# Performance work log

Measured on AMD Instinct MI355X. Metric: run time of the kernel, lower is better.

The kernel has to match this reference:

```python
import jax, jax.numpy as jnp
import numpy as np

N_TOKENS = 7168
EMBED_DIM = 256
N_HEADS = 8
HEAD_DIM = EMBED_DIM // N_HEADS  # 32
HALF = HEAD_DIM // 2             # 16 rotary frequency pairs per head
BATCH = 4
MAX_LEN = 2048
POSITION_DIM = 2
N_LEVELS = 4
LN_EPS = 1e-5
SPATIAL_THETA = 100.0
LEVEL_THETA = 10.0


def setup_inputs() -> dict:
    key = jax.random.key(0)
    ks = jax.random.split(key, 6)
    x = jax.random.normal(ks[0], (N_TOKENS, EMBED_DIM), jnp.float32)
    level_indices = jax.random.randint(ks[1], (N_TOKENS,), 0, N_LEVELS, dtype=jnp.int32)
    level_spatial_shapes = jnp.array([[32, 32], [16, 16], [8, 8], [4, 4]], jnp.int32)
    # positions in each token's own level coordinate space
    u = jax.random.uniform(ks[2], (N_TOKENS, POSITION_DIM), jnp.float32)
    spatial_positions = u * level_spatial_shapes[level_indices].astype(jnp.float32)
    # ragged batch boundaries: lengths [2048, 1536, 2048, 1536]
    batch_offsets = jnp.array([0, 2048, 3584, 5632, 7168], jnp.int32)
    ln_w = jnp.ones((EMBED_DIM,), jnp.float32)
    ln_b = jnp.zeros((EMBED_DIM,), jnp.float32)
    qkv_w = jax.random.normal(ks[3], (3 * EMBED_DIM, EMBED_DIM), jnp.float32) * (EMBED_DIM ** -0.5)
    out_w = jax.random.normal(ks[4], (EMBED_DIM, EMBED_DIM), jnp.float32) * (EMBED_DIM ** -0.5)
    # ND-RoPE frequencies: (position_dim+1, n_heads, head_dim//2).
    # Spatial dims share magnitude theta_s^(-i/HALF) split over a random per-head
    # direction angle; level dim uses theta_l^(-i/HALF).
    mag_s = SPATIAL_THETA ** (-jnp.arange(HALF, dtype=jnp.float32) / HALF)
    mag_l = LEVEL_THETA ** (-jnp.arange(HALF, dtype=jnp.float32) / HALF)
    phi = jax.random.uniform(ks[5], (N_HEADS, HALF), jnp.float32) * (2.0 * jnp.pi)
    freqs = jnp.stack([mag_s * jnp.cos(phi),
                       mag_s * jnp.sin(phi),
                       jnp.broadcast_to(mag_l, (N_HEADS, HALF))], axis=0)
    return {"x": x, "spatial_positions": spatial_positions,
            "level_indices": level_indices, "level_spatial_shapes": level_spatial_shapes,
            "batch_offsets": batch_offsets, "ln_w": ln_w, "ln_b": ln_b,
            "qkv_w": qkv_w, "out_w": out_w, "freqs": freqs}


def reference(x, spatial_positions, level_indices, level_spatial_shapes,
              batch_offsets, ln_w, ln_b, qkv_w, out_w, freqs):
    residual = x
    # pre-norm LayerNorm
    mu = jnp.mean(x, -1, keepdims=True)
    var = jnp.mean((x - mu) ** 2, -1, keepdims=True)
    xn = (x - mu) * jax.lax.rsqrt(var + LN_EPS) * ln_w + ln_b
    q, k, v = jnp.split(xn @ qkv_w.T, 3, axis=-1)  # each (N, E)
    # prep_multilevel_positions: rescale each level to the max level's coordinate
    # frame and append the level index as an extra position dim.
    shapes_tok = level_spatial_shapes[level_indices].astype(jnp.float32)  # (N, 2)
    max_shape = jnp.max(level_spatial_shapes, axis=0).astype(jnp.float32)  # (2,)
    pos = jnp.concatenate([spatial_positions * (max_shape / shapes_tok),
                           level_indices[:, None].astype(jnp.float32)], axis=-1)  # (N, 3)
    # per-head ND RoPE: angle = sum_d pos_d * freq_d
    theta = jnp.einsum('nd,dhf->nhf', pos, freqs)  # (N, H, HALF)
    cos, sin = jnp.cos(theta), jnp.sin(theta)

    def rope(t):
        t = t.reshape(N_TOKENS, N_HEADS, HALF, 2)
        r = jnp.stack([t[..., 0] * cos - t[..., 1] * sin,
                       t[..., 0] * sin + t[..., 1] * cos], axis=-1)
        return r.reshape(N_TOKENS, EMBED_DIM)

    q, k = rope(q), rope(k)
    # concatenated -> padded (B, S, E)
    tok = jnp.arange(N_TOKENS)
    b_of = jnp.searchsorted(batch_offsets, tok, side='right') - 1  # (N,) batch index
    p_of = tok - batch_offsets[b_of]                               # (N,) pos in batch
    lens = batch_offsets[1:] - batch_offsets[:-1]
    pad_mask = jnp.arange(MAX_LEN)[None, :] >= lens[:, None]  # (B, S), True = padding

    def heads(t):
        padded = jnp.zeros((BATCH, MAX_LEN, EMBED_DIM), t.dtype).at[b_of, p_of].set(t)
        return padded.reshape(BATCH, MAX_LEN, N_HEADS, HEAD_DIM).transpose(0, 2, 1, 3)

    qh, kh, vh = heads(q), heads(k), heads(v)  # (B, H, S, hd)
    scores = jnp.einsum('bhqd,bhkd->bhqk', qh, kh) / np.float32(np.sqrt(HEAD_DIM))
    scores = jnp.where(pad_mask[:, None, None, :], jnp.float32(-1e9), scores)
    attn = jax.nn.softmax(scores, axis=-1)
    out = jnp.einsum('bhqk,bhkd->bhqd', attn, vh)
    out = out.transpose(0, 2, 1, 3).reshape(BATCH, MAX_LEN, EMBED_DIM)
    out_cat = out[b_of, p_of]  # padded -> concatenated (padded rows dropped)
    return out_cat @ out_w.T + residual
```

## Files before the change

### kernel.cpp

```cpp
#include <hip/hip_runtime.h>
#include <hip/hip_bf16.h>

#define NT   7168
#define ED   256
#define NH   8
#define HD   32
#define HF   16
#define QKVN 768
#define QSCL 0.25503471600819466f

typedef float f32x4  __attribute__((ext_vector_type(4)));
typedef __bf16 bf16x8 __attribute__((ext_vector_type(8)));

__device__ __forceinline__ short f2bf(float f) {
    union { float f; unsigned u; } v; v.f = f;
    unsigned r = v.u + 0x7FFFu + ((v.u >> 16) & 1u);
    return (short)(r >> 16);
}
__device__ __forceinline__ float fexp2(float x) {
    float r; asm("v_exp_f32 %0, %1" : "=v"(r) : "v"(x)); return r;
}
__device__ __forceinline__ unsigned cvtpk(float lo, float hi) {
    unsigned r; asm("v_cvt_pk_bf16_f32 %0, %1, %2" : "=v"(r) : "v"(lo), "v"(hi)); return r;
}
__device__ __forceinline__ float bf2f(short s) {
    union { unsigned u; float f; } v; v.u = ((unsigned)(unsigned short)s) << 16;
    return v.f;
}
__device__ __forceinline__ unsigned pack2bf(float a, float b) {
    union { float f; unsigned u; } ua, ub; ua.f = a; ub.f = b;
    return ((ua.u + 0x8000u) >> 16) | ((ub.u + 0x8000u) & 0xFFFF0000u);
}
__device__ __forceinline__ void gll16(const void* g, void* l) {
    __builtin_amdgcn_global_load_lds((const __attribute__((address_space(1))) void*)g,
                                     (__attribute__((address_space(3))) void*)l, 16, 0, 0);
}

__global__ __launch_bounds__(256) void ln_conv_kernel(const float* __restrict__ x,
                                                      const float* __restrict__ w,
                                                      const float* __restrict__ b,
                                                      short* __restrict__ xn,
                                                      const float* __restrict__ qkvw,
                                                      const float* __restrict__ outw,
                                                      short* __restrict__ wq,
                                                      short* __restrict__ wo,
                                                      const float* __restrict__ sp,
                                                      const int* __restrict__ lvl,
                                                      const int* __restrict__ shp,
                                                      const float* __restrict__ freqs,
                                                      unsigned* __restrict__ tab) {
    int bid = blockIdx.x;
    int tid = threadIdx.x;
    if (bid >= NT / 4) {
        int i = (bid - NT / 4) * 256 + tid;
        if (i < QKVN * ED) wq[i] = f2bf(qkvw[i]);
        if (i < ED * ED)   wo[i] = f2bf(outw[i]);
        return;
    }
    int tok  = bid * 4 + (tid >> 6);
    int lane = tid & 63;
    const float4 xv = *reinterpret_cast<const float4*>(x + tok * ED + lane * 4);
    float s  = xv.x + xv.y + xv.z + xv.w;
    float ss = xv.x * xv.x + xv.y * xv.y + xv.z * xv.z + xv.w * xv.w;
#pragma unroll
    for (int m = 1; m < 64; m <<= 1) { s += __shfl_xor(s, m); ss += __shfl_xor(ss, m); }
    float mu  = s * (1.0f / ED);
    float inv = rsqrtf(ss * (1.0f / ED) - mu * mu + 1e-5f);
    const float4 wv = *reinterpret_cast<const float4*>(w + lane * 4);
    const float4 bv = *reinterpret_cast<const float4*>(b + lane * 4);
    short4 o;
    o.x = f2bf((xv.x - mu) * inv * wv.x + bv.x);
    o.y = f2bf((xv.y - mu) * inv * wv.y + bv.y);
    o.z = f2bf((xv.z - mu) * inv * wv.z + bv.z);
    o.w = f2bf((xv.w - mu) * inv * wv.w + bv.w);
    *reinterpret_cast<short4*>(xn + tok * ED + lane * 4) = o;

    int tt = bid * 4 + (tid >> 6);
    int h  = (tid >> 3) & 7;
    int f  = (tid & 7) * 2;
    int L = lvl[tt];
    float mx0 = fmaxf(fmaxf((float)shp[0], (float)shp[2]), fmaxf((float)shp[4], (float)shp[6]));
    float mx1 = fmaxf(fmaxf((float)shp[1], (float)shp[3]), fmaxf((float)shp[5], (float)shp[7]));
    float p0 = sp[tt * 2]     * (mx0 / (float)shp[L * 2]);
    float p1 = sp[tt * 2 + 1] * (mx1 / (float)shp[L * 2 + 1]);
    float p2 = (float)L;
    int fi = h * HF + f;
    float th0 = p0 * freqs[fi]       + p1 * freqs[128 + fi]       + p2 * freqs[256 + fi];
    float th1 = p0 * freqs[fi + 1]   + p1 * freqs[128 + fi + 1]   + p2 * freqs[256 + fi + 1];
    float sn0, cs0, sn1, cs1;
    __sincosf(th0, &sn0, &cs0);
    __sincosf(th1, &sn1, &cs1);
    uint2 pk;
    pk.x = pack2bf(cs0, sn0);
    pk.y = pack2bf(cs1, sn1);
    *reinterpret_cast<uint2*>(&tab[tt * 128 + fi]) = pk;
}

__global__ __launch_bounds__(256) void gemm_qkv(const short* __restrict__ A,
                                                const short* __restrict__ B,
                                                short* __restrict__ C,
                                                const unsigned* __restrict__ tab,
                                                short* __restrict__ vt) {
    __shared__ __align__(16) short tile[4][2560];
    int wv = threadIdx.x >> 6, lane = threadIdx.x & 63;
    int r = lane & 15, g = lane >> 4;
    int mt = blockIdx.x * 128 + wv * 32;
    int jt = blockIdx.y * 64;
    const short* arow0 = A + (mt + r) * ED + g * 8;
    const short* arow1 = A + (mt + 16 + r) * ED + g * 8;
    const short* brow  = B + (jt + r) * ED + g * 8;
    f32x4 acc0[4] = {{0,0,0,0},{0,0,0,0},{0,0,0,0},{0,0,0,0}};
    f32x4 acc1[4] = {{0,0,0,0},{0,0,0,0},{0,0,0,0},{0,0,0,0}};
#pragma unroll
    for (int k0 = 0; k0 < ED; k0 += 32) {
        bf16x8 a0 = *reinterpret_cast<const bf16x8*>(arow0 + k0);
        bf16x8 a1 = *reinterpret_cast<const bf16x8*>(arow1 + k0);
#pragma unroll
        for (int c = 0; c < 4; ++c) {
            bf16x8 bb = *reinterpret_cast<const bf16x8*>(brow + c * 16 * ED + k0);
            acc0[c] = __builtin_amdgcn_mfma_f32_16x16x32_bf16(a0, bb, acc0[c], 0, 0, 0);
            acc1[c] = __builtin_amdgcn_mfma_f32_16x16x32_bf16(a1, bb, acc1[c], 0, 0, 0);
        }
    }
    short* tl = tile[wv];
    if (jt < 512) {
        const float qs = (jt < 256) ? QSCL : 1.0f;
        const int odd = r & 1;
#pragma unroll
        for (int c = 0; c < 4; ++c) {
            int col = jt + c * 16 + r;
            int hf = ((col >> 5) & 7) * 16 + ((col >> 1) & 15);
#pragma unroll
            for (int rr = 0; rr < 4; ++rr) {
                int t0 = mt + g * 4 + rr;
                unsigned pk0 = tab[t0 * 128 + hf];
                float cs0 = bf2f((short)(pk0 & 0xFFFF)), sn0 = bf2f((short)(pk0 >> 16));
                float v0 = acc0[c][rr], p0 = __shfl_xor(v0, 1);
                float o0 = (odd ? (v0 * cs0 + p0 * sn0) : (v0 * cs0 - p0 * sn0)) * qs;
                int t1 = t0 + 16;
                unsigned pk1 = tab[t1 * 128 + hf];
                float cs1 = bf2f((short)(pk1 & 0xFFFF)), sn1 = bf2f((short)(pk1 >> 16));
                float v1 = acc1[c][rr], p1 = __shfl_xor(v1, 1);
                float o1 = (odd ? (v1 * cs1 + p1 * sn1) : (v1 * cs1 - p1 * sn1)) * qs;
                float n0 = __shfl_xor(o0, 1);
                float n1 = __shfl_xor(o1, 1);
                int tok = (odd ? 16 : 0) + g * 4 + rr;
                unsigned dw = odd ? pack2bf(n1, o1) : pack2bf(o0, n0);
                int colw = c * 16 + (r & ~1);
                *reinterpret_cast<unsigned*>(&tl[tok * 72 + colw]) = dw;
            }
        }
#pragma unroll
        for (int p2 = 0; p2 < 4; ++p2) {
            int tok = p2 * 8 + (lane >> 3), chunk = lane & 7;
            uint4 d = *reinterpret_cast<const uint4*>(&tl[tok * 72 + chunk * 8]);
            *reinterpret_cast<uint4*>(&C[(size_t)(mt + tok) * QKVN + jt + chunk * 8]) = d;
        }
    } else {
#pragma unroll
        for (int c = 0; c < 4; ++c) {
            int row = c * 16 + r;
#pragma unroll
            for (int rr = 0; rr < 4; rr += 2) {
                unsigned d0 = pack2bf(acc0[c][rr], acc0[c][rr + 1]);
                unsigned d1 = pack2bf(acc1[c][rr], acc1[c][rr + 1]);
                *reinterpret_cast<unsigned*>(&tl[row * 40 + rr + 8 * g])     = d0;
                *reinterpret_cast<unsigned*>(&tl[row * 40 + rr + 4 + 8 * g]) = d1;
            }
        }
#pragma unroll
        for (int p2 = 0; p2 < 4; ++p2) {
            int dim = p2 * 16 + (lane >> 2), chunk = lane & 3;
            uint4 d = *reinterpret_cast<const uint4*>(&tl[dim * 40 + chunk * 8]);
            *reinterpret_cast<uint4*>(&vt[(size_t)(jt - 512 + dim) * NT + mt + chunk * 8]) = d;
        }
    }
}

__global__ __launch_bounds__(256) void gemm_out(const short* __restrict__ A,
                                                const short* __restrict__ B,
                                                const float* __restrict__ res,
                                                float* __restrict__ out) {
    int wv = threadIdx.x >> 6, lane = threadIdx.x & 63;
    int r = lane & 15, g = lane >> 4;
    int mt = blockIdx.x * 64 + wv * 16;
    int jt = blockIdx.y * 64;
    const short* arow = A + (mt + r) * ED + g * 8;
    const short* brow = B + (jt + r) * ED + g * 8;
    f32x4 acc[4] = {{0,0,0,0},{0,0,0,0},{0,0,0,0},{0,0,0,0}};
#pragma unroll
    for (int k0 = 0; k0 < ED; k0 += 32) {
        bf16x8 a = *reinterpret_cast<const bf16x8*>(arow + k0);
#pragma unroll
        for (int c = 0; c < 4; ++c) {
            bf16x8 bb = *reinterpret_cast<const bf16x8*>(brow + c * 16 * ED + k0);
            acc[c] = __builtin_amdgcn_mfma_f32_16x16x32_bf16(a, bb, acc[c], 0, 0, 0);
        }
    }
#pragma unroll
    for (int c = 0; c < 4; ++c)
#pragma unroll
        for (int rr = 0; rr < 4; ++rr) {
            int idx = (mt + g * 4 + rr) * ED + jt + c * 16 + r;
            out[idx] = acc[c][rr] + res[idx];
        }
}

__global__ __launch_bounds__(512) void attn_kernel(const short* __restrict__ qkv,
                                                   const short* __restrict__ vt,
                                                   short* __restrict__ obf) {
    __shared__ __align__(16) short smem[32768];
    const int tid = threadIdx.x;
    const int wv = tid >> 6, lane = tid & 63;
    const int bid = blockIdx.x;
    const int h = bid & 7, pr = bid >> 3;
    const int b = (pr >= 16) + (pr >= 28) + (pr >= 44);
    const int off = (b == 0) ? 0 : (b == 1) ? 2048 : (b == 2) ? 3584 : 5632;
    const int len = (b == 0) ? 2048 : (b == 1) ? 1536 : (b == 2) ? 2048 : 1536;
    const int pb  = (b == 0) ? 0 : (b == 1) ? 16 : (b == 2) ? 28 : 44;
    const int q0 = off + (pr - pb) * 128;
    const int r = lane & 15, g = lane >> 4;
    const int qi = wv & 3, half = wv >> 2;
    const int hl = len >> 1;
    const int nst = hl >> 7;
    const int qs = q0 + qi * 32;

    const int sh = tid >> 8, inner = tid & 255;
    const short* pK0 = qkv + ED + h * HD + (size_t)(off + sh * hl + (inner >> 2)) * QKVN + (inner & 3) * 8;
    const short* pV0 = vt + (size_t)(h * HD + ((inner >> 2) & 31)) * NT + off + sh * hl + (inner >> 7) * 32 + (inner & 3) * 8;
    const int dK0 = sh * 4096 + inner * 8;
    const int dK1 = sh * 4096 + (inner + 256) * 8;
    const int dV0 = 8192 + sh * 4096 + inner * 8;
    const int dV1 = 8192 + sh * 4096 + 2048 + inner * 8;

#define STAGE(B, s) { \
        const short* k_ = pK0 + (size_t)(s) * 128 * QKVN; \
        gll16(k_,             &smem[(B) * 16384 + dK0]); \
        gll16(k_ + 64 * QKVN, &smem[(B) * 16384 + dK1]); \
        const short* v_ = pV0 + (s) * 128; \
        gll16(v_,      &smem[(B) * 16384 + dV0]); \
        gll16(v_ + 64, &smem[(B) * 16384 + dV1]); }

    bf16x8 qfA = *reinterpret_cast<const bf16x8*>(qkv + (size_t)(qs + r) * QKVN + h * HD + g * 8);
    bf16x8 qfB = *reinterpret_cast<const bf16x8*>(qkv + (size_t)(qs + 16 + r) * QKVN + h * HD + g * 8);
    union { unsigned u[4]; bf16x8 v; } onesu;
    onesu.u[0] = onesu.u[1] = onesu.u[2] = onesu.u[3] = 0x3F803F80u;
    const bf16x8 ones = onesu.v;

    f32x4 o0A = {0,0,0,0}, o1A = {0,0,0,0}, o0B = {0,0,0,0}, o1B = {0,0,0,0};
    f32x4 olA = {0,0,0,0}, olB = {0,0,0,0};

    STAGE(0, 0);
    __syncthreads();

    for (int st = 0; st < nst; ++st) {
        const int Bb = st & 1;
        if (st + 1 < nst) STAGE(Bb ^ 1, st + 1);
#pragma unroll
        for (int sub = 0; sub < 2; ++sub) {
            const short* kl = &smem[Bb * 16384 + half * 4096 + sub * 2048];
            const short* vl = &smem[Bb * 16384 + 8192 + half * 4096 + sub * 2048];
            bf16x8 kf0 = *reinterpret_cast<const bf16x8*>(kl +        r * 32 + g * 8);
            bf16x8 kf1 = *reinterpret_cast<const bf16x8*>(kl +  512 + r * 32 + g * 8);
            bf16x8 kf2 = *reinterpret_cast<const bf16x8*>(kl + 1024 + r * 32 + g * 8);
            bf16x8 kf3 = *reinterpret_cast<const bf16x8*>(kl + 1536 + r * 32 + g * 8);
            bf16x8 v00 = *reinterpret_cast<const bf16x8*>(vl +        r * 32 + g * 8);
            bf16x8 v10 = *reinterpret_cast<const bf16x8*>(vl +  512 + r * 32 + g * 8);
            bf16x8 v01 = *reinterpret_cast<const bf16x8*>(vl + 1024 + r * 32 + g * 8);
            bf16x8 v11 = *reinterpret_cast<const bf16x8*>(vl + 1536 + r * 32 + g * 8);

            const f32x4 z = {0, 0, 0, 0};
            __builtin_amdgcn_s_setprio(1);
            f32x4 sA0 = __builtin_amdgcn_mfma_f32_16x16x32_bf16(kf0, qfA, z, 0, 0, 0);
            f32x4 sA1 = __builtin_amdgcn_mfma_f32_16x16x32_bf16(kf1, qfA, z, 0, 0, 0);
            f32x4 sA2 = __builtin_amdgcn_mfma_f32_16x16x32_bf16(kf2, qfA, z, 0, 0, 0);
            f32x4 sA3 = __builtin_amdgcn_mfma_f32_16x16x32_bf16(kf3, qfA, z, 0, 0, 0);
            f32x4 sB0 = __builtin_amdgcn_mfma_f32_16x16x32_bf16(kf0, qfB, z, 0, 0, 0);
            f32x4 sB1 = __builtin_amdgcn_mfma_f32_16x16x32_bf16(kf1, qfB, z, 0, 0, 0);
            f32x4 sB2 = __builtin_amdgcn_mfma_f32_16x16x32_bf16(kf2, qfB, z, 0, 0, 0);
            f32x4 sB3 = __builtin_amdgcn_mfma_f32_16x16x32_bf16(kf3, qfB, z, 0, 0, 0);
            __builtin_amdgcn_s_setprio(0);

#pragma unroll
            for (int i = 0; i < 4; ++i) {
                sA0[i] = fexp2(sA0[i]); sA1[i] = fexp2(sA1[i]);
                sA2[i] = fexp2(sA2[i]); sA3[i] = fexp2(sA3[i]);
                sB0[i] = fexp2(sB0[i]); sB1[i] = fexp2(sB1[i]);
                sB2[i] = fexp2(sB2[i]); sB3[i] = fexp2(sB3[i]);
            }
            union { unsigned u[4]; bf16x8 v; } pA0, pA1, pB0, pB1;
            pA0.u[0] = cvtpk(sA0[0], sA0[1]); pA0.u[1] = cvtpk(sA0[2], sA0[3]);
            pA0.u[2] = cvtpk(sA1[0], sA1[1]); pA0.u[3] = cvtpk(sA1[2], sA1[3]);
            pA1.u[0] = cvtpk(sA2[0], sA2[1]); pA1.u[1] = cvtpk(sA2[2], sA2[3]);
            pA1.u[2] = cvtpk(sA3[0], sA3[1]); pA1.u[3] = cvtpk(sA3[2], sA3[3]);
            pB0.u[0] = cvtpk(sB0[0], sB0[1]); pB0.u[1] = cvtpk(sB0[2], sB0[3]);
            pB0.u[2] = cvtpk(sB1[0], sB1[1]); pB0.u[3] = cvtpk(sB1[2], sB1[3]);
            pB1.u[0] = cvtpk(sB2[0], sB2[1]); pB1.u[1] = cvtpk(sB2[2], sB2[3]);
            pB1.u[2] = cvtpk(sB3[0], sB3[1]); pB1.u[3] = cvtpk(sB3[2], sB3[3]);
            __builtin_amdgcn_s_setprio(1);
            o0A = __builtin_amdgcn_mfma_f32_16x16x32_bf16(v00, pA0.v, o0A, 0, 0, 0);
            o0A = __builtin_amdgcn_mfma_f32_16x16x32_bf16(v01, pA1.v, o0A, 0, 0, 0);
            o1A = __builtin_amdgcn_mfma_f32_16x16x32_bf16(v10, pA0.v, o1A, 0, 0, 0);
            o1A = __builtin_amdgcn_mfma_f32_16x16x32_bf16(v11, pA1.v, o1A, 0, 0, 0);
            o0B = __builtin_amdgcn_mfma_f32_16x16x32_bf16(v00, pB0.v, o0B, 0, 0, 0);
            o0B = __builtin_amdgcn_mfma_f32_16x16x32_bf16(v01, pB1.v, o0B, 0, 0, 0);
            o1B = __builtin_amdgcn_mfma_f32_16x16x32_bf16(v10, pB0.v, o1B, 0, 0, 0);
            o1B = __builtin_amdgcn_mfma_f32_16x16x32_bf16(v11, pB1.v, o1B, 0, 0, 0);
            olA = __builtin_amdgcn_mfma_f32_16x16x32_bf16(ones, pA0.v, olA, 0, 0, 0);
            olA = __builtin_amdgcn_mfma_f32_16x16x32_bf16(ones, pA1.v, olA, 0, 0, 0);
            olB = __builtin_amdgcn_mfma_f32_16x16x32_bf16(ones, pB0.v, olB, 0, 0, 0);
            olB = __builtin_amdgcn_mfma_f32_16x16x32_bf16(ones, pB1.v, olB, 0, 0, 0);
            __builtin_amdgcn_s_setprio(0);
        }
        __syncthreads();
    }

    float lA = olA[0], lB = olB[0];

    float* cf = (float*)smem + (qi * 64 + lane) * 19;
    if (half) {
#pragma unroll
        for (int i = 0; i < 4; ++i) {
            cf[i] = o0A[i]; cf[4 + i] = o1A[i]; cf[8 + i] = o0B[i]; cf[12 + i] = o1B[i];
        }
        cf[16] = lA; cf[17] = lB;
    }
    __syncthreads();
    if (!half) {
        lA += cf[16]; lB += cf[17];
#pragma unroll
        for (int i = 0; i < 4; ++i) {
            o0A[i] += cf[i];     o1A[i] += cf[4 + i];
            o0B[i] += cf[8 + i]; o1B[i] += cf[12 + i];
        }
        float iA = 1.f / lA, iB = 1.f / lB;
        short4 w;
        short* orowA = obf + (qs + r) * ED + h * HD;
        w.x = f2bf(o0A[0] * iA); w.y = f2bf(o0A[1] * iA);
        w.z = f2bf(o0A[2] * iA); w.w = f2bf(o0A[3] * iA);
        *reinterpret_cast<short4*>(orowA + g * 4) = w;
        w.x = f2bf(o1A[0] * iA); w.y = f2bf(o1A[1] * iA);
        w.z = f2bf(o1A[2] * iA); w.w = f2bf(o1A[3] * iA);
        *reinterpret_cast<short4*>(orowA + 16 + g * 4) = w;
        short* orowB = obf + (qs + 16 + r) * ED + h * HD;
        w.x = f2bf(o0B[0] * iB); w.y = f2bf(o0B[1] * iB);
        w.z = f2bf(o0B[2] * iB); w.w = f2bf(o0B[3] * iB);
        *reinterpret_cast<short4*>(orowB + g * 4) = w;
        w.x = f2bf(o1B[0] * iB); w.y = f2bf(o1B[1] * iB);
        w.z = f2bf(o1B[2] * iB); w.w = f2bf(o1B[3] * iB);
        *reinterpret_cast<short4*>(orowB + 16 + g * 4) = w;
    }
#undef STAGE
}

extern "C" void kernel_launch(void* const* d_in, const int* in_sizes, int n_in,
                              void* d_out, int out_size, void* d_ws, size_t ws_size,
                              hipStream_t stream) {
    const float* x     = (const float*)d_in[0];
    const float* sp    = (const float*)d_in[1];
    const int*   lvl   = (const int*)d_in[2];
    const int*   shp   = (const int*)d_in[3];
    const float* lnw   = (const float*)d_in[5];
    const float* lnb   = (const float*)d_in[6];
    const float* qkvw  = (const float*)d_in[7];
    const float* outw  = (const float*)d_in[8];
    const float* freqs = (const float*)d_in[9];
    float* out = (float*)d_out;

    char* ws = (char*)d_ws;
    short* xn  = (short*)ws; ws += NT * ED * 2;
    short* qkv = (short*)ws; ws += NT * QKVN * 2;
    short* vt  = (short*)ws; ws += ED * NT * 2;
    short* obf = (short*)ws; ws += NT * ED * 2;
    short* wq  = (short*)ws; ws += QKVN * ED * 2;
    short* wo  = (short*)ws; ws += ED * ED * 2;
    unsigned* tab = (unsigned*)ws; ws += NT * 128 * 4;

    ln_conv_kernel<<<dim3(NT / 4 + 768), dim3(256), 0, stream>>>(
        x, lnw, lnb, xn, qkvw, outw, wq, wo, sp, lvl, shp, freqs, tab);
    gemm_qkv<<<dim3(NT / 128, QKVN / 64), dim3(256), 0, stream>>>(xn, wq, qkv, tab, vt);
    attn_kernel<<<dim3(56 * 8), dim3(512), 0, stream>>>(qkv, vt, obf);
    gemm_out<<<dim3(NT / 64, ED / 64), dim3(256), 0, stream>>>(obf, wo, x, out);
}
```

Measured before the change: 67.71 us.

## Re-split attention waves into 64-query tiles over key quarters with VALU row sums

The attention block now splits its 8 waves as 2 query groups of 64 rows times 4 key quarters, instead of 4 groups of 32 rows times 2 key halves. Each stage stages 64 keys, so every K/V fragment read from LDS feeds twice as many queries. The softmax denominator is now accumulated with VALU adds and cross-lane shuffles rather than extra MFMAs against a ones vector. The price is more accumulator registers per wave, a larger three-way LDS reduction at the end, and a min-occupancy launch bound that may constrain register allocation.

```diff
diff --git a/kernel.cpp b/kernel.cpp
--- a/kernel.cpp
+++ b/kernel.cpp
@@ -30,6 +30,9 @@
 __device__ __forceinline__ unsigned pack2bf(float a, float b) {
     union { float f; unsigned u; } ua, ub; ua.f = a; ub.f = b;
     return ((ua.u + 0x8000u) >> 16) | ((ub.u + 0x8000u) & 0xFFFF0000u);
+}
+__device__ __forceinline__ float vsum4(f32x4 v) {
+    return (v[0] + v[1]) + (v[2] + v[3]);
 }
 __device__ __forceinline__ void gll16(const void* g, void* l) {
     __builtin_amdgcn_global_load_lds((const __attribute__((address_space(1))) void*)g,
@@ -206,9 +209,9 @@
         }
 }
 
-__global__ __launch_bounds__(512) void attn_kernel(const short* __restrict__ qkv,
-                                                   const short* __restrict__ vt,
-                                                   short* __restrict__ obf) {
+__global__ __launch_bounds__(512, 4) void attn_kernel(const short* __restrict__ qkv,
+                                                      const short* __restrict__ vt,
+                                                      short* __restrict__ obf) {
     __shared__ __align__(16) short smem[32768];
     const int tid = threadIdx.x;
     const int wv = tid >> 6, lane = tid & 63;
@@ -220,35 +223,34 @@
     const int pb  = (b == 0) ? 0 : (b == 1) ? 16 : (b == 2) ? 28 : 44;
     const int q0 = off + (pr - pb) * 128;
     const int r = lane & 15, g = lane >> 4;
-    const int qi = wv & 3, half = wv >> 2;
-    const int hl = len >> 1;
-    const int nst = hl >> 7;
-    const int qs = q0 + qi * 32;
-
-    const int sh = tid >> 8, inner = tid & 255;
-    const short* pK0 = qkv + ED + h * HD + (size_t)(off + sh * hl + (inner >> 2)) * QKVN + (inner & 3) * 8;
-    const short* pV0 = vt + (size_t)(h * HD + ((inner >> 2) & 31)) * NT + off + sh * hl + (inner >> 7) * 32 + (inner & 3) * 8;
-    const int dK0 = sh * 4096 + inner * 8;
-    const int dK1 = sh * 4096 + (inner + 256) * 8;
-    const int dV0 = 8192 + sh * 4096 + inner * 8;
-    const int dV1 = 8192 + sh * 4096 + 2048 + inner * 8;
+    const int qi = wv & 1, qr = wv >> 1;
+    const int ql = len >> 2;
+    const int nst = ql >> 6;
+    const int qs = q0 + qi * 64;
+
+    const int qr_s = tid >> 7, inner = tid & 127;
+    const short* pK = qkv + ED + h * HD + (size_t)(off + qr_s * ql + (inner >> 2)) * QKVN + (inner & 3) * 8;
+    const short* pV = vt + (size_t)(h * HD + (inner >> 2)) * NT + off + qr_s * ql + (inner & 3) * 8;
+    const int dK = qr_s * 4096 + inner * 8;
+    const int dV = dK + 2048;
 
 #define STAGE(B, s) { \
-        const short* k_ = pK0 + (size_t)(s) * 128 * QKVN; \
-        gll16(k_,             &smem[(B) * 16384 + dK0]); \
-        gll16(k_ + 64 * QKVN, &smem[(B) * 16384 + dK1]); \
-        const short* v_ = pV0 + (s) * 128; \
-        gll16(v_,      &smem[(B) * 16384 + dV0]); \
-        gll16(v_ + 64, &smem[(B) * 16384 + dV1]); }
-
-    bf16x8 qfA = *reinterpret_cast<const bf16x8*>(qkv + (size_t)(qs + r) * QKVN + h * HD + g * 8);
-    bf16x8 qfB = *reinterpret_cast<const bf16x8*>(qkv + (size_t)(qs + 16 + r) * QKVN + h * HD + g * 8);
-    union { unsigned u[4]; bf16x8 v; } onesu;
-    onesu.u[0] = onesu.u[1] = onesu.u[2] = onesu.u[3] = 0x3F803F80u;
-    const bf16x8 ones = onesu.v;
-
-    f32x4 o0A = {0,0,0,0}, o1A = {0,0,0,0}, o0B = {0,0,0,0}, o1B = {0,0,0,0};
-    f32x4 olA = {0,0,0,0}, olB = {0,0,0,0};
+        const short* k_ = pK + (size_t)(s) * 64 * QKVN; \
+        gll16(k_,             &smem[(B) * 16384 + dK]); \
+        gll16(k_ + 32 * QKVN, &smem[(B) * 16384 + dK + 1024]); \
+        const short* v_ = pV + (s) * 64; \
+        gll16(v_,      &smem[(B) * 16384 + dV]); \
+        gll16(v_ + 32, &smem[(B) * 16384 + dV + 1024]); }
+
+    const short* qbase = qkv + (size_t)(qs + r) * QKVN + h * HD + g * 8;
+    bf16x8 qf0 = *reinterpret_cast<const bf16x8*>(qbase);
+    bf16x8 qf1 = *reinterpret_cast<const bf16x8*>(qbase + 16 * QKVN);
+    bf16x8 qf2 = *reinterpret_cast<const bf16x8*>(qbase + 32 * QKVN);
+    bf16x8 qf3 = *reinterpret_cast<const bf16x8*>(qbase + 48 * QKVN);
+
+    f32x4 o00 = {0,0,0,0}, o01 = {0,0,0,0}, o10 = {0,0,0,0}, o11 = {0,0,0,0};
+    f32x4 o20 = {0,0,0,0}, o21 = {0,0,0,0}, o30 = {0,0,0,0}, o31 = {0,0,0,0};
+    float l0 = 0.f, l1 = 0.f, l2 = 0.f, l3 = 0.f;
 
     STAGE(0, 0);
     __syncthreads();
@@ -256,31 +258,29 @@
     for (int st = 0; st < nst; ++st) {
         const int Bb = st & 1;
         if (st + 1 < nst) STAGE(Bb ^ 1, st + 1);
-#pragma unroll
-        for (int sub = 0; sub < 2; ++sub) {
-            const short* kl = &smem[Bb * 16384 + half * 4096 + sub * 2048];
-            const short* vl = &smem[Bb * 16384 + 8192 + half * 4096 + sub * 2048];
-            bf16x8 kf0 = *reinterpret_cast<const bf16x8*>(kl +        r * 32 + g * 8);
-            bf16x8 kf1 = *reinterpret_cast<const bf16x8*>(kl +  512 + r * 32 + g * 8);
-            bf16x8 kf2 = *reinterpret_cast<const bf16x8*>(kl + 1024 + r * 32 + g * 8);
-            bf16x8 kf3 = *reinterpret_cast<const bf16x8*>(kl + 1536 + r * 32 + g * 8);
-            bf16x8 v00 = *reinterpret_cast<const bf16x8*>(vl +        r * 32 + g * 8);
-            bf16x8 v10 = *reinterpret_cast<const bf16x8*>(vl +  512 + r * 32 + g * 8);
-            bf16x8 v01 = *reinterpret_cast<const bf16x8*>(vl + 1024 + r * 32 + g * 8);
-            bf16x8 v11 = *reinterpret_cast<const bf16x8*>(vl + 1536 + r * 32 + g * 8);
-
-            const f32x4 z = {0, 0, 0, 0};
+        const short* kl = &smem[Bb * 16384 + qr * 4096];
+        const short* vl = kl + 2048;
+        bf16x8 kf0 = *reinterpret_cast<const bf16x8*>(kl +        r * 32 + g * 8);
+        bf16x8 kf1 = *reinterpret_cast<const bf16x8*>(kl +  512 + r * 32 + g * 8);
+        bf16x8 kf2 = *reinterpret_cast<const bf16x8*>(kl + 1024 + r * 32 + g * 8);
+        bf16x8 kf3 = *reinterpret_cast<const bf16x8*>(kl + 1536 + r * 32 + g * 8);
+        bf16x8 v00 = *reinterpret_cast<const bf16x8*>(vl +        r * 32 + g * 8);
+        bf16x8 v10 = *reinterpret_cast<const bf16x8*>(vl +  512 + r * 32 + g * 8);
+        bf16x8 v01 = *reinterpret_cast<const bf16x8*>(vl + 1024 + r * 32 + g * 8);
+        bf16x8 v11 = *reinterpret_cast<const bf16x8*>(vl + 1536 + r * 32 + g * 8);
+        const f32x4 z = {0, 0, 0, 0};
+
+        {
             __builtin_amdgcn_s_setprio(1);
-            f32x4 sA0 = __builtin_amdgcn_mfma_f32_16x16x32_bf16(kf0, qfA, z, 0, 0, 0);
-            f32x4 sA1 = __builtin_amdgcn_mfma_f32_16x16x32_bf16(kf1, qfA, z, 0, 0, 0);
-            f32x4 sA2 = __builtin_amdgcn_mfma_f32_16x16x32_bf16(kf2, qfA, z, 0, 0, 0);
-            f32x4 sA3 = __builtin_amdgcn_mfma_f32_16x16x32_bf16(kf3, qfA, z, 0, 0, 0);
-            f32x4 sB0 = __builtin_amdgcn_mfma_f32_16x16x32_bf16(kf0, qfB, z, 0, 0, 0);
-            f32x4 sB1 = __builtin_amdgcn_mfma_f32_16x16x32_bf16(kf1, qfB, z, 0, 0, 0);
-            f32x4 sB2 = __builtin_amdgcn_mfma_f32_16x16x32_bf16(kf2, qfB, z, 0, 0, 0);
-            f32x4 sB3 = __builtin_amdgcn_mfma_f32_16x16x32_bf16(kf3, qfB, z, 0, 0, 0);
+            f32x4 sA0 = __builtin_amdgcn_mfma_f32_16x16x32_bf16(kf0, qf0, z, 0, 0, 0);
+            f32x4 sA1 = __builtin_amdgcn_mfma_f32_16x16x32_bf16(kf1, qf0, z, 0, 0, 0);
+            f32x4 sA2 = __builtin_amdgcn_mfma_f32_16x16x32_bf16(kf2, qf0, z, 0, 0, 0);
+            f32x4 sA3 = __builtin_amdgcn_mfma_f32_16x16x32_bf16(kf3, qf0, z, 0, 0, 0);
+            f32x4 sB0 = __builtin_amdgcn_mfma_f32_16x16x32_bf16(kf0, qf1, z, 0, 0, 0);
+            f32x4 sB1 = __builtin_amdgcn_mfma_f32_16x16x32_bf16(kf1, qf1, z, 0, 0, 0);
+            f32x4 sB2 = __builtin_amdgcn_mfma_f32_16x16x32_bf16(kf2, qf1, z, 0, 0, 0);
+            f32x4 sB3 = __builtin_amdgcn_mfma_f32_16x16x32_bf16(kf3, qf1, z, 0, 0, 0);
             __builtin_amdgcn_s_setprio(0);
-
 #pragma unroll
             for (int i = 0; i < 4; ++i) {
                 sA0[i] = fexp2(sA0[i]); sA1[i] = fexp2(sA1[i]);
@@ -288,6 +288,8 @@
                 sB0[i] = fexp2(sB0[i]); sB1[i] = fexp2(sB1[i]);
                 sB2[i] = fexp2(sB2[i]); sB3[i] = fexp2(sB3[i]);
             }
+            l0 += (vsum4(sA0) + vsum4(sA1)) + (vsum4(sA2) + vsum4(sA3));
+            l1 += (vsum4(sB0) + vsum4(sB1)) + (vsum4(sB2) + vsum4(sB3));
             union { unsigned u[4]; bf16x8 v; } pA0, pA1, pB0, pB1;
             pA0.u[0] = cvtpk(sA0[0], sA0[1]); pA0.u[1] = cvtpk(sA0[2], sA0[3]);
             pA0.u[2] = cvtpk(sA1[0], sA1[1]); pA0.u[3] = cvtpk(sA1[2], sA1[3]);
@@ -298,57 +300,103 @@
             pB1.u[0] = cvtpk(sB2[0], sB2[1]); pB1.u[1] = cvtpk(sB2[2], sB2[3]);
             pB1.u[2] = cvtpk(sB3[0], sB3[1]); pB1.u[3] = cvtpk(sB3[2], sB3[3]);
             __builtin_amdgcn_s_setprio(1);
-            o0A = __builtin_amdgcn_mfma_f32_16x16x32_bf16(v00, pA0.v, o0A, 0, 0, 0);
-            o0A = __builtin_amdgcn_mfma_f32_16x16x32_bf16(v01, pA1.v, o0A, 0, 0, 0);
-            o1A = __builtin_amdgcn_mfma_f32_16x16x32_bf16(v10, pA0.v, o1A, 0, 0, 0);
-            o1A = __builtin_amdgcn_mfma_f32_16x16x32_bf16(v11, pA1.v, o1A, 0, 0, 0);
-            o0B = __builtin_amdgcn_mfma_f32_16x16x32_bf16(v00, pB0.v, o0B, 0, 0, 0);
-            o0B = __builtin_amdgcn_mfma_f32_16x16x32_bf16(v01, pB1.v, o0B, 0, 0, 0);
-            o1B = __builtin_amdgcn_mfma_f32_16x16x32_bf16(v10, pB0.v, o1B, 0, 0, 0);
-            o1B = __builtin_amdgcn_mfma_f32_16x16x32_bf16(v11, pB1.v, o1B, 0, 0, 0);
-            olA = __builtin_amdgcn_mfma_f32_16x16x32_bf16(ones, pA0.v, olA, 0, 0, 0);
-            olA = __builtin_amdgcn_mfma_f32_16x16x32_bf16(ones, pA1.v, olA, 0, 0, 0);
-            olB = __builtin_amdgcn_mfma_f32_16x16x32_bf16(ones, pB0.v, olB, 0, 0, 0);
-            olB = __builtin_amdgcn_mfma_f32_16x16x32_bf16(ones, pB1.v, olB, 0, 0, 0);
+            o00 = __builtin_amdgcn_mfma_f32_16x16x32_bf16(v00, pA0.v, o00, 0, 0, 0);
+            o00 = __builtin_amdgcn_mfma_f32_16x16x32_bf16(v01, pA1.v, o00, 0, 0, 0);
+            o01 = __builtin_amdgcn_mfma_f32_16x16x32_bf16(v10, pA0.v, o01, 0, 0, 0);
+            o01 = __builtin_amdgcn_mfma_f32_16x16x32_bf16(v11, pA1.v, o01, 0, 0, 0);
+            o10 = __builtin_amdgcn_mfma_f32_16x16x32_bf16(v00, pB0.v, o10, 0, 0, 0);
+            o10 = __builtin_amdgcn_mfma_f32_16x16x32_bf16(v01, pB1.v, o10, 0, 0, 0);
+            o11 = __builtin_amdgcn_mfma_f32_16x16x32_bf16(v10, pB0.v, o11, 0, 0, 0);
+            o11 = __builtin_amdgcn_mfma_f32_16x16x32_bf16(v11, pB1.v, o11, 0, 0, 0);
             __builtin_amdgcn_s_setprio(0);
         }
+        {
+            __builtin_amdgcn_s_setprio(1);
+            f32x4 sA0 = __builtin_amdgcn_mfma_f32_16x16x32_bf16(kf0, qf2, z, 0, 0, 0);
+            f32x4 sA1 = __builtin_amdgcn_mfma_f32_16x16x32_bf16(kf1, qf2, z, 0, 0, 0);
+            f32x4 sA2 = __builtin_amdgcn_mfma_f32_16x16x32_bf16(kf2, qf2, z, 0, 0, 0);
+            f32x4 sA3 = __builtin_amdgcn_mfma_f32_16x16x32_bf16(kf3, qf2, z, 0, 0, 0);
+            f32x4 sB0 = __builtin_amdgcn_mfma_f32_16x16x32_bf16(kf0, qf3, z, 0, 0, 0);
+            f32x4 sB1 = __builtin_amdgcn_mfma_f32_16x16x32_bf16(kf1, qf3, z, 0, 0, 0);
+            f32x4 sB2 = __builtin_amdgcn_mfma_f32_16x16x32_bf16(kf2, qf3, z, 0, 0, 0);
+            f32x4 sB3 = __builtin_amdgcn_mfma_f32_16x16x32_bf16(kf3, qf3, z, 0, 0, 0);
+            __builtin_amdgcn_s_setprio(0);
+#pragma unroll
+            for (int i = 0; i < 4; ++i) {
+                sA0[i] = fexp2(sA0[i]); sA1[i] = fexp2(sA1[i]);
+                sA2[i] = fexp2(sA2[i]); sA3[i] = fexp2(sA3[i]);
+                sB0[i] = fexp2(sB0[i]); sB1[i] = fexp2(sB1[i]);
+                sB2[i] = fexp2(sB2[i]); sB3[i] = fexp2(sB3[i]);
+            }
+            l2 += (vsum4(sA0) + vsum4(sA1)) + (vsum4(sA2) + vsum4(sA3));
+            l3 += (vsum4(sB0) + vsum4(sB1)) + (vsum4(sB2) + vsum4(sB3));
+            union { unsigned u[4]; bf16x8 v; } pA0, pA1, pB0, pB1;
+            pA0.u[0] = cvtpk(sA0[0], sA0[1]); pA0.u[1] = cvtpk(sA0[2], sA0[3]);
+            pA0.u[2] = cvtpk(sA1[0], sA1[1]); pA0.u[3] = cvtpk(sA1[2], sA1[3]);
+            pA1.u[0] = cvtpk(sA2[0], sA2[1]); pA1.u[1] = cvtpk(sA2[2], sA2[3]);
+            pA1.u[2] = cvtpk(sA3[0], sA3[1]); pA1.u[3] = cvtpk(sA3[2], sA3[3]);
+            pB0.u[0] = cvtpk(sB0[0], sB0[1]); pB0.u[1] = cvtpk(sB0[2], sB0[3]);
+            pB0.u[2] = cvtpk(sB1[0], sB1[1]); pB0.u[3] = cvtpk(sB1[2], sB1[3]);
+            pB1.u[0] = cvtpk(sB2[0], sB2[1]); pB1.u[1] = cvtpk(sB2[2], sB2[3]);
+            pB1.u[2] = cvtpk(sB3[0], sB3[1]); pB1.u[3] = cvtpk(sB3[2], sB3[3]);
+            __builtin_amdgcn_s_setprio(1);
+            o20 = __builtin_amdgcn_mfma_f32_16x16x32_bf16(v00, pA0.v, o20, 0, 0, 0);
+            o20 = __builtin_amdgcn_mfma_f32_16x16x32_bf16(v01, pA1.v, o20, 0, 0, 0);
+            o21 = __builtin_amdgcn_mfma_f32_16x16x32_bf16(v10, pA0.v, o21, 0, 0, 0);
+            o21 = __builtin_amdgcn_mfma_f32_16x16x32_bf16(v11, pA1.v, o21, 0, 0, 0);
+            o30 = __builtin_amdgcn_mfma_f32_16x16x32_bf16(v00, pB0.v, o30, 0, 0, 0);
+            o30 = __builtin_amdgcn_mfma_f32_16x16x32_bf16(v01, pB1.v, o30, 0, 0, 0);
+            o31 = __builtin_amdgcn_mfma_f32_16x16x32_bf16(v10, pB0.v, o31, 0, 0, 0);
+            o31 = __builtin_amdgcn_mfma_f32_16x16x32_bf16(v11, pB1.v, o31, 0, 0, 0);
+            __builtin_amdgcn_s_setprio(0);
+        }
         __syncthreads();
     }
 
-    float lA = olA[0], lB = olB[0];
-
-    float* cf = (float*)smem + (qi * 64 + lane) * 19;
-    if (half) {
+    if (qr) {
+        float* cf = (float*)smem + ((qi * 3 + (qr - 1)) * 64 + lane) * 36;
 #pragma unroll
         for (int i = 0; i < 4; ++i) {
-            cf[i] = o0A[i]; cf[4 + i] = o1A[i]; cf[8 + i] = o0B[i]; cf[12 + i] = o1B[i];
-        }
-        cf[16] = lA; cf[17] = lB;
+            cf[i]      = o00[i]; cf[4 + i]  = o01[i];
+            cf[8 + i]  = o10[i]; cf[12 + i] = o11[i];
+            cf[16 + i] = o20[i]; cf[20 + i] = o21[i];
+            cf[24 + i] = o30[i]; cf[28 + i] = o31[i];
+        }
+        cf[32] = l0; cf[33] = l1; cf[34] = l2; cf[35] = l3;
     }
     __syncthreads();
-    if (!half) {
-        lA += cf[16]; lB += cf[17];
-#pragma unroll
-        for (int i = 0; i < 4; ++i) {
-            o0A[i] += cf[i];     o1A[i] += cf[4 + i];
-            o0B[i] += cf[8 + i]; o1B[i] += cf[12 + i];
-        }
-        float iA = 1.f / lA, iB = 1.f / lB;
+    if (qr == 0) {
+#pragma unroll
+        for (int w = 0; w < 3; ++w) {
+            const float* cf = (float*)smem + ((qi * 3 + w) * 64 + lane) * 36;
+#pragma unroll
+            for (int i = 0; i < 4; ++i) {
+                o00[i] += cf[i];      o01[i] += cf[4 + i];
+                o10[i] += cf[8 + i];  o11[i] += cf[12 + i];
+                o20[i] += cf[16 + i]; o21[i] += cf[20 + i];
+                o30[i] += cf[24 + i]; o31[i] += cf[28 + i];
+            }
+            l0 += cf[32]; l1 += cf[33]; l2 += cf[34]; l3 += cf[35];
+        }
+        l0 += __shfl_xor(l0, 16); l0 += __shfl_xor(l0, 32);
+        l1 += __shfl_xor(l1, 16); l1 += __shfl_xor(l1, 32);
+        l2 += __shfl_xor(l2, 16); l2 += __shfl_xor(l2, 32);
+        l3 += __shfl_xor(l3, 16); l3 += __shfl_xor(l3, 32);
+        float i0 = 1.f / l0, i1 = 1.f / l1, i2 = 1.f / l2, i3 = 1.f / l3;
         short4 w;
-        short* orowA = obf + (qs + r) * ED + h * HD;
-        w.x = f2bf(o0A[0] * iA); w.y = f2bf(o0A[1] * iA);
-        w.z = f2bf(o0A[2] * iA); w.w = f2bf(o0A[3] * iA);
-        *reinterpret_cast<short4*>(orowA + g * 4) = w;
-        w.x = f2bf(o1A[0] * iA); w.y = f2bf(o1A[1] * iA);
-        w.z = f2bf(o1A[2] * iA); w.w = f2bf(o1A[3] * iA);
-        *reinterpret_cast<short4*>(orowA + 16 + g * 4) = w;
-        short* orowB = obf + (qs + 16 + r) * ED + h * HD;
-        w.x = f2bf(o0B[0] * iB); w.y = f2bf(o0B[1] * iB);
-        w.z = f2bf(o0B[2] * iB); w.w = f2bf(o0B[3] * iB);
-        *reinterpret_cast<short4*>(orowB + g * 4) = w;
-        w.x = f2bf(o1B[0] * iB); w.y = f2bf(o1B[1] * iB);
-        w.z = f2bf(o1B[2] * iB); w.w = f2bf(o1B[3] * iB);
-        *reinterpret_cast<short4*>(orowB + 16 + g * 4) = w;
+        short* orow = obf + (size_t)(qs + r) * ED + h * HD;
+#define WROW(of0, of1, iv, roff) { \
+        w.x = f2bf(of0[0] * iv); w.y = f2bf(of0[1] * iv); \
+        w.z = f2bf(of0[2] * iv); w.w = f2bf(of0[3] * iv); \
+        *reinterpret_cast<short4*>(orow + (size_t)(roff) * ED + g * 4) = w; \
+        w.x = f2bf(of1[0] * iv); w.y = f2bf(of1[1] * iv); \
+        w.z = f2bf(of1[2] * iv); w.w = f2bf(of1[3] * iv); \
+        *reinterpret_cast<short4*>(orow + (size_t)(roff) * ED + 16 + g * 4) = w; }
+        WROW(o00, o01, i0, 0);
+        WROW(o10, o11, i1, 16);
+        WROW(o20, o21, i2, 32);
+        WROW(o30, o31, i3, 48);
+#undef WROW
     }
 #undef STAGE
 }
```

Result: slower. 98.49 us (+45.5%).
